# Performance work log

Measured on AMD Instinct MI355X. Metric: run time of the kernel, lower is better.

## Reference

```python
import jax, jax.numpy as jnp
import numpy as np

ATTRACTION_W = 1.0
REPULSION_W = 1.0
BETA_POS_W = 1.0
BETA_NEG_W = 0.5
K_INST = 256  # max number of distinct instance ids (slice ids)


def setup_inputs() -> dict:
    key = jax.random.key(0)
    B, N, D, K = 4, 65536, 256, K_INST
    k1, k2, k3 = jax.random.split(key, 3)
    beta = jax.random.normal(k1, (B, N, 1), jnp.float32)
    embed = jax.random.normal(k2, (B, N, D), jnp.float32)
    sid = jax.random.randint(k3, (B, N), -1, K)  # -1 = background
    # force exactly one condensation point per instance: hit i (<K) -> sid=i, is_cp
    sid = sid.at[:, :K].set(jnp.broadcast_to(jnp.arange(K), (B, K)))
    is_cp = jnp.zeros((B, N), bool).at[:, :K].set(True)
    return {"beta": beta, "embed": embed, "slice_id": sid, "is_cp": is_cp}


def _loss_single(beta, emb, sid, cp):
    # beta: (N,) logits, emb: (N,D), sid: (N,) int, cp: (N,) bool
    N = sid.shape[0]
    valid = sid >= 0
    cpv = cp & valid  # condensation points with a valid instance id
    # BCE-with-logits: target 1 -> softplus(-x), target 0 -> softplus(x)
    pos = jnp.sum(jnp.where(cpv, jax.nn.softplus(-beta), 0.0)) / jnp.maximum(cpv.sum(), 1)
    noncp = ~cp
    neg = jnp.sum(jnp.where(noncp, jax.nn.softplus(beta), 0.0)) / jnp.maximum(noncp.sum(), 1)
    beta_loss = BETA_POS_W * pos + BETA_NEG_W * neg

    # first CP hit index per instance (segment-min over CP hits), N = "no CP"
    sid_c = jnp.where(valid, sid, 0)
    idx = jnp.arange(N)
    first_cp = jnp.full((K_INST,), N, jnp.int32).at[sid_c].min(
        jnp.where(cpv, idx, N).astype(jnp.int32))
    has_cp = first_cp < N
    cp_emb = emb[jnp.minimum(first_cp, N - 1)]  # (K, D), garbage where no CP

    # attraction: sum over instances of mean ||emb - inst_cp||^2
    d2 = jnp.sum((emb - cp_emb[sid_c]) ** 2, axis=-1)  # (N,)
    w = valid & has_cp[sid_c]
    seg_sum = jnp.zeros((K_INST,), jnp.float32).at[sid_c].add(jnp.where(w, d2, 0.0))
    seg_cnt = jnp.zeros((K_INST,), jnp.float32).at[sid_c].add(w.astype(jnp.float32))
    attraction = jnp.sum(jnp.where(seg_cnt > 0, seg_sum / jnp.maximum(seg_cnt, 1.0), 0.0))
    attraction = attraction * ATTRACTION_W

    # repulsion: mean exp(-||cp_i - cp_j||^2) over all CP pairs (incl. diagonal)
    pd2 = jnp.sum((cp_emb[:, None, :] - cp_emb[None, :, :]) ** 2, axis=-1)  # (K,K)
    pmask = has_cp[:, None] & has_cp[None, :]
    M = has_cp.sum()
    rep = jnp.sum(jnp.where(pmask, jnp.exp(-pd2), 0.0)) / jnp.maximum(M * M, 1)
    rep = jnp.where(M > 1, rep * REPULSION_W, 0.0)

    loss = beta_loss + attraction + rep
    ok = (valid.sum() > 0) & (cpv.sum() > 0)
    return jnp.where(ok, loss, 0.0), ok


def reference(beta, embed, slice_id, is_cp):
    losses, oks = jax.vmap(_loss_single)(beta.squeeze(-1), embed, slice_id, is_cp)
    cnt = oks.sum()
    return jnp.where(cnt > 0, losses.sum() / jnp.maximum(cnt, 1), 0.0)
```

## Files before the change

kernel.cpp:

```cpp
#include <hip/hip_runtime.h>
#include <math.h>

#define K_INST 256
#define ATTRACTION_W 1.0f
#define REPULSION_W 1.0f
#define BETA_POS_W 1.0f
#define BETA_NEG_W 0.5f

typedef float f32x4 __attribute__((ext_vector_type(4)));
typedef int i32x4 __attribute__((ext_vector_type(4)));

__device__ inline float softplusf(float x) {
    return fmaxf(x, 0.f) + log1pf(expf(-fabsf(x)));
}

__device__ inline float waveReduceSumF(float v) {
    for (int o = 32; o; o >>= 1) v += __shfl_xor(v, o);
    return v;
}
__device__ inline int waveReduceSumI(int v) {
    for (int o = 32; o; o >>= 1) v += __shfl_xor(v, o);
    return v;
}

__global__ void stats_kernel(const float* __restrict__ beta,
                             const int* __restrict__ sid,
                             const int* __restrict__ is_cp,
                             int* fc_rev,
                             float* pos_sum, float* neg_sum,
                             int* seg_cnt,
                             int* cpv_cnt, int* noncp_cnt, int* valid_cnt,
                             int N) {
    int b = blockIdx.y;
    int base = (blockIdx.x * blockDim.x + threadIdx.x) * 4;
    const float* betaB = beta + (size_t)b * N;
    const int* sidB = sid + (size_t)b * N;
    const int* cpB = is_cp + (size_t)b * N;

    __shared__ int hist[K_INST];
    for (int k = threadIdx.x; k < K_INST; k += blockDim.x) hist[k] = 0;
    __syncthreads();

    i32x4 s4 = *(const i32x4*)(sidB + base);
    i32x4 c4 = *(const i32x4*)(cpB + base);
    f32x4 x4 = *(const f32x4*)(betaB + base);

    float pos = 0.f, neg = 0.f;
    int c_cpv = 0, c_non = 0, c_val = 0;
    #pragma unroll
    for (int e = 0; e < 4; ++e) {
        int s = s4[e], cp = c4[e];
        float x = x4[e];
        bool valid = s >= 0;
        bool cpv = cp && valid;
        if (valid) atomicAdd(&hist[s], 1);
        if (cpv) {
            pos += softplusf(-x);
            c_cpv++;
            atomicMax(&fc_rev[b * K_INST + s], N - (base + e));
        }
        if (!cp) {
            neg += softplusf(x);
            c_non++;
        }
        c_val += valid ? 1 : 0;
    }

    __shared__ float sf[2][4];
    __shared__ int si[3][4];
    pos = waveReduceSumF(pos);
    neg = waveReduceSumF(neg);
    c_cpv = waveReduceSumI(c_cpv);
    c_non = waveReduceSumI(c_non);
    c_val = waveReduceSumI(c_val);
    int wave = threadIdx.x >> 6, lane = threadIdx.x & 63;
    if (lane == 0) {
        sf[0][wave] = pos; sf[1][wave] = neg;
        si[0][wave] = c_cpv; si[1][wave] = c_non; si[2][wave] = c_val;
    }
    __syncthreads();
    if (threadIdx.x == 0) {
        float p = sf[0][0] + sf[0][1] + sf[0][2] + sf[0][3];
        float n = sf[1][0] + sf[1][1] + sf[1][2] + sf[1][3];
        int a = si[0][0] + si[0][1] + si[0][2] + si[0][3];
        int c = si[1][0] + si[1][1] + si[1][2] + si[1][3];
        int v = si[2][0] + si[2][1] + si[2][2] + si[2][3];
        if (p != 0.f) atomicAdd(&pos_sum[b], p);
        if (n != 0.f) atomicAdd(&neg_sum[b], n);
        if (a) atomicAdd(&cpv_cnt[b], a);
        if (c) atomicAdd(&noncp_cnt[b], c);
        if (v) atomicAdd(&valid_cnt[b], v);
    }
    for (int k = threadIdx.x; k < K_INST; k += blockDim.x) {
        int h = hist[k];
        if (h) atomicAdd(&seg_cnt[b * K_INST + k], h);
    }
}

__global__ void scatter_kernel(const int* __restrict__ sid,
                               const int* __restrict__ seg_cnt,
                               int* cursor, int* order, int N) {
    int b = blockIdx.y;
    int base = (blockIdx.x * blockDim.x + threadIdx.x) * 4;
    const int* sidB = sid + (size_t)b * N;
    int* orderB = order + (size_t)b * N;

    __shared__ int lhist[K_INST];
    __shared__ int lcnt[K_INST];
    __shared__ int lbase[K_INST];
    __shared__ int scanA[K_INST];
    __shared__ int scanB[K_INST];

    int t = threadIdx.x;
    lhist[t] = 0; lcnt[t] = 0;
    __syncthreads();

    i32x4 s4 = *(const i32x4*)(sidB + base);
    #pragma unroll
    for (int e = 0; e < 4; ++e) {
        if (s4[e] >= 0) atomicAdd(&lhist[s4[e]], 1);
    }
    __syncthreads();

    int myCnt = seg_cnt[b * K_INST + t];
    scanA[t] = myCnt;
    __syncthreads();
    int* src = scanA; int* dst = scanB;
    #pragma unroll
    for (int off = 1; off < K_INST; off <<= 1) {
        int v = src[t] + ((t >= off) ? src[t - off] : 0);
        dst[t] = v;
        __syncthreads();
        int* tmp = src; src = dst; dst = tmp;
    }
    int segStart = src[t] - myCnt;
    int h = lhist[t];
    lbase[t] = (h > 0) ? atomicAdd(&cursor[b * K_INST + t], h) : 0;
    __syncthreads();

    #pragma unroll
    for (int e = 0; e < 4; ++e) {
        int s = s4[e];
        if (s >= 0) {
            int r = atomicAdd(&lcnt[s], 1);
        }
    }
    scanA[t] = segStart;
    __syncthreads();
    lcnt[t] = 0;
    __syncthreads();
    #pragma unroll
    for (int e = 0; e < 4; ++e) {
        int s = s4[e];
        if (s >= 0) {
            int r = atomicAdd(&lcnt[s], 1);
            int slot = scanA[s] + lbase[s] + r;
            orderB[slot] = ((base + e) << 8) | s;
        }
    }
}

__global__ void gather_kernel(const float* __restrict__ embed,
                              const int* __restrict__ fc_rev,
                              float* __restrict__ cp_emb,
                              float* __restrict__ cp_embT, int N) {
    int b = blockIdx.y;
    int k = blockIdx.x;
    int src = N - fc_rev[b * K_INST + k];
    if (src >= N) src = N - 1;
    int lane = threadIdx.x;
    const float* embB = embed + (size_t)b * N * 256;
    f32x4 v = ((const f32x4*)(embB + (size_t)src * 256))[lane];
    ((f32x4*)(cp_emb + ((size_t)b * K_INST + k) * 256))[lane] = v;
    float* T = cp_embT + (size_t)b * K_INST * 256;
    int d = lane * 4;
    T[(size_t)(d + 0) * 256 + k] = v[0];
    T[(size_t)(d + 1) * 256 + k] = v[1];
    T[(size_t)(d + 2) * 256 + k] = v[2];
    T[(size_t)(d + 3) * 256 + k] = v[3];
}

__device__ inline float sel8f(const float* v, int lane) {
    float a0 = (lane & 1) ? v[1] : v[0];
    float a1 = (lane & 1) ? v[3] : v[2];
    float a2 = (lane & 1) ? v[5] : v[4];
    float a3 = (lane & 1) ? v[7] : v[6];
    float b0 = (lane & 2) ? a1 : a0;
    float b1 = (lane & 2) ? a3 : a2;
    return (lane & 4) ? b1 : b0;
}
__device__ inline int sel8i(const int* v, int lane) {
    int a0 = (lane & 1) ? v[1] : v[0];
    int a1 = (lane & 1) ? v[3] : v[2];
    int a2 = (lane & 1) ? v[5] : v[4];
    int a3 = (lane & 1) ? v[7] : v[6];
    int b0 = (lane & 2) ? a1 : a0;
    int b1 = (lane & 2) ? a3 : a2;
    return (lane & 4) ? b1 : b0;
}

__global__ void attraction_repulsion_kernel(
        const float* __restrict__ embed,
        const int* __restrict__ order,
        const int* __restrict__ fc_rev,
        const float* __restrict__ cp_emb,
        const float* __restrict__ cp_embT,
        float* seg_sum, float* rep_sum,
        int N, int atr_blocks) {
    int b = blockIdx.y;
    __shared__ __align__(16) char smem[8448];
    __shared__ float sf[4];

    const float* cpB = cp_emb + (size_t)b * K_INST * 256;

    if (blockIdx.x < 32) {
        float (*srow)[264] = (float(*)[264])smem;
        const int* fcB = fc_rev + b * K_INST;
        int i0 = blockIdx.x * 8;
        const float* T = cp_embT + (size_t)b * K_INST * 256;
        {
            int r = threadIdx.x >> 5, cc = (threadIdx.x & 31) * 8;
            f32x4 a = *(const f32x4*)(cpB + (size_t)(i0 + r) * 256 + cc);
            f32x4 bv = *(const f32x4*)(cpB + (size_t)(i0 + r) * 256 + cc + 4);
            srow[r][cc + 0] = a[0]; srow[r][cc + 1] = a[1];
            srow[r][cc + 2] = a[2]; srow[r][cc + 3] = a[3];
            srow[r][cc + 4] = bv[0]; srow[r][cc + 5] = bv[1];
            srow[r][cc + 6] = bv[2]; srow[r][cc + 7] = bv[3];
        }
        __syncthreads();

        int j = threadIdx.x;
        bool has_j = fcB[j] > 0;
        float acc[8] = {0.f, 0.f, 0.f, 0.f, 0.f, 0.f, 0.f, 0.f};
        for (int d = 0; d < 256; d += 2) {
            float v0 = T[(size_t)d * 256 + j];
            float v1 = T[(size_t)(d + 1) * 256 + j];
            #pragma unroll
            for (int r = 0; r < 8; ++r) {
                float f0 = srow[r][d] - v0;
                float f1 = srow[r][d + 1] - v1;
                acc[r] += f0 * f0 + f1 * f1;
            }
        }
        float val = 0.f;
        #pragma unroll
        for (int r = 0; r < 8; ++r) {
            bool has_i = fcB[i0 + r] > 0;
            if (has_i && has_j) val += expf(-acc[r]);
        }
        val = waveReduceSumF(val);
        int wave = threadIdx.x >> 6, lane = threadIdx.x & 63;
        if (lane == 0) sf[wave] = val;
        __syncthreads();
        if (threadIdx.x == 0)
            atomicAdd(&rep_sum[b], sf[0] + sf[1] + sf[2] + sf[3]);
    } else {
        float* s_sum = (float*)smem;
        for (int k = threadIdx.x; k < K_INST; k += blockDim.x) s_sum[k] = 0.f;
        __syncthreads();

        int bx = blockIdx.x - 32;
        int lane = threadIdx.x & 63;
        int wid = bx * 4 + (threadIdx.x >> 6);
        int stride = atr_blocks * 4 * 8;

        const float* embB = embed + (size_t)b * N * 256;
        const int* ordB = order + (size_t)b * N;

        int i = wid * 8;
        i32x4 ea = {-1, -1, -1, -1}, eb = {-1, -1, -1, -1};
        if (i < N) {
            ea = __builtin_nontemporal_load((const i32x4*)(ordB + i));
            eb = __builtin_nontemporal_load((const i32x4*)(ordB + i + 4));
        }
        while (i < N) {
            int en[8] = {ea[0], ea[1], ea[2], ea[3], eb[0], eb[1], eb[2], eb[3]};
            int ss[8];
            #pragma unroll
            for (int j = 0; j < 8; ++j) ss[j] = en[j] < 0 ? -1 : (en[j] & 255);

            f32x4 e[8];
            #pragma unroll
            for (int j = 0; j < 8; ++j) {
                int off = ((en[j] < 0 ? 0 : (en[j] >> 8)) << 8) | (lane << 2);
                e[j] = __builtin_nontemporal_load((const f32x4*)(embB + off));
            }
            f32x4 c[8];
            #pragma unroll
            for (int j = 0; j < 8; ++j) {
                int off = ((ss[j] < 0 ? 0 : ss[j]) << 8) | (lane << 2);
                c[j] = *(const f32x4*)(cpB + off);
            }
            int inext = i + stride;
            i32x4 na = {-1, -1, -1, -1}, nb = {-1, -1, -1, -1};
            if (inext < N) {
                na = __builtin_nontemporal_load((const i32x4*)(ordB + inext));
                nb = __builtin_nontemporal_load((const i32x4*)(ordB + inext + 4));
            }

            float v[8];
            #pragma unroll
            for (int j = 0; j < 8; ++j) {
                float d0 = e[j][0] - c[j][0], d1 = e[j][1] - c[j][1];
                float d2 = e[j][2] - c[j][2], d3 = e[j][3] - c[j][3];
                v[j] = d0 * d0 + d1 * d1 + d2 * d2 + d3 * d3;
            }
            #pragma unroll
            for (int o = 1; o <= 4; o <<= 1) {
                #pragma unroll
                for (int j = 0; j < 8; ++j) v[j] += __shfl_xor(v[j], o);
            }
            float w = sel8f(v, lane & 7);
            #pragma unroll
            for (int o = 8; o <= 32; o <<= 1) w += __shfl_xor(w, o);
            if (lane < 8) {
                int s_sel = sel8i(ss, lane);
                if (s_sel >= 0) atomicAdd(&s_sum[s_sel], w);
            }
            ea = na; eb = nb;
            i = inext;
        }
        __syncthreads();
        for (int k = threadIdx.x; k < K_INST; k += blockDim.x) {
            float v = s_sum[k];
            if (v != 0.f) atomicAdd(&seg_sum[b * K_INST + k], v);
        }
    }
}

__global__ void final_kernel(const int* __restrict__ fc_rev,
                             const float* __restrict__ seg_sum,
                             const int* __restrict__ seg_cnt,
                             const float* __restrict__ pos_sum,
                             const float* __restrict__ neg_sum,
                             const float* __restrict__ rep_sum,
                             const int* __restrict__ cpv_cnt,
                             const int* __restrict__ noncp_cnt,
                             const int* __restrict__ valid_cnt,
                             float* out, int N, int B) {
    __shared__ float s_att[4];
    __shared__ int s_m[4];
    float loss_sum = 0.f;
    int ok_cnt = 0;
    int wave = threadIdx.x >> 6, lane = threadIdx.x & 63;
    for (int b = 0; b < B; ++b) {
        int k = threadIdx.x;
        int has = (fc_rev[b * K_INST + k] > 0) ? 1 : 0;
        int cnt = seg_cnt[b * K_INST + k];
        float att = (has && cnt > 0) ? (seg_sum[b * K_INST + k] / (float)cnt) : 0.f;
        att = waveReduceSumF(att);
        has = waveReduceSumI(has);
        if (lane == 0) { s_att[wave] = att; s_m[wave] = has; }
        __syncthreads();
        if (threadIdx.x == 0) {
            float attraction = (s_att[0] + s_att[1] + s_att[2] + s_att[3]) * ATTRACTION_W;
            int M = s_m[0] + s_m[1] + s_m[2] + s_m[3];
            float pos = pos_sum[b] / fmaxf((float)cpv_cnt[b], 1.f);
            float neg = neg_sum[b] / fmaxf((float)noncp_cnt[b], 1.f);
            float beta_loss = BETA_POS_W * pos + BETA_NEG_W * neg;
            float rep = 0.f;
            if (M > 1) {
                float mm = (float)M * (float)M;
                rep = (rep_sum[b] / fmaxf(mm, 1.f)) * REPULSION_W;
            }
            float loss = beta_loss + attraction + rep;
            bool ok = (valid_cnt[b] > 0) && (cpv_cnt[b] > 0);
            if (ok) { loss_sum += loss; ok_cnt += 1; }
        }
        __syncthreads();
    }
    if (threadIdx.x == 0) {
        out[0] = (ok_cnt > 0) ? (loss_sum / (float)ok_cnt) : 0.f;
    }
}

extern "C" void kernel_launch(void* const* d_in, const int* in_sizes, int n_in,
                              void* d_out, int out_size, void* d_ws, size_t ws_size,
                              hipStream_t stream) {
    const float* beta  = (const float*)d_in[0];
    const float* embed = (const float*)d_in[1];
    const int* sid     = (const int*)d_in[2];
    const int* is_cp   = (const int*)d_in[3];
    float* out = (float*)d_out;

    const int N = 65536;
    const int B = in_sizes[0] / N;
    (void)n_in; (void)out_size; (void)ws_size;

    char* ws = (char*)d_ws;
    int*   fc_rev    = (int*)(ws + 0);
    float* seg_sum   = (float*)(ws + 4096);
    int*   seg_cnt   = (int*)(ws + 8192);
    int*   cursor    = (int*)(ws + 12288);
    float* pos_sum   = (float*)(ws + 16384);
    float* neg_sum   = (float*)(ws + 16448);
    float* rep_sum   = (float*)(ws + 16512);
    int*   cpv_cnt   = (int*)(ws + 16576);
    int*   noncp_cnt = (int*)(ws + 16640);
    int*   valid_cnt = (int*)(ws + 16704);
    int*   order     = (int*)(ws + 20480);
    float* cp_emb    = (float*)(ws + 20480 + (size_t)B * N * 4);
    float* cp_embT   = cp_emb + (size_t)B * K_INST * 256;

    hipMemsetAsync(ws, 0, 20480, stream);
    hipMemsetAsync(order, 0xFF, (size_t)B * N * 4, stream);

    stats_kernel<<<dim3(N / 1024, B), dim3(256), 0, stream>>>(
        beta, sid, is_cp, fc_rev, pos_sum, neg_sum, seg_cnt,
        cpv_cnt, noncp_cnt, valid_cnt, N);

    scatter_kernel<<<dim3(N / 1024, B), dim3(256), 0, stream>>>(
        sid, seg_cnt, cursor, order, N);

    gather_kernel<<<dim3(K_INST, B), dim3(64), 0, stream>>>(
        embed, fc_rev, cp_emb, cp_embT, N);

    const int atr_blocks = 512;
    attraction_repulsion_kernel<<<dim3(32 + atr_blocks, B), dim3(256), 0, stream>>>(
        embed, order, fc_rev, cp_emb, cp_embT,
        seg_sum, rep_sum, N, atr_blocks);

    final_kernel<<<dim3(1), dim3(256), 0, stream>>>(
        fc_rev, seg_sum, seg_cnt, pos_sum, neg_sum, rep_sum,
        cpv_cnt, noncp_cnt, valid_cnt, out, N, B);
}
```

Baseline: 105.0 us.

## Compute attraction per segment via sum and sum-of-squares expansion

Attraction is now computed with one block per instance. Each block walks that instance's sorted hit list and accumulates the vector sum and the sum of squares of the embeddings. The mean squared distance then comes from the expansion ||e||^2 - 2 e·c + ||c||^2, so no per-hit CP embedding load or shuffle reduction is needed. The repulsion blocks are widened to 512 threads covering 16 rows each, the order-buffer fill memset is removed, and the scatter kernel drops its second counting pass. The cost is possible load imbalance across segments, a short serial loop per wave, and cancellation error in float32 from the expanded form.

```diff
diff --git a/kernel.cpp b/kernel.cpp
--- a/kernel.cpp
+++ b/kernel.cpp
@@ -99,7 +99,7 @@
 
 __global__ void scatter_kernel(const int* __restrict__ sid,
                                const int* __restrict__ seg_cnt,
-                               int* cursor, int* order, int N) {
+                               int* cursor, int* order, int* seg_start, int N) {
     int b = blockIdx.y;
     int base = (blockIdx.x * blockDim.x + threadIdx.x) * 4;
     const int* sidB = sid + (size_t)b * N;
@@ -110,6 +110,7 @@
     __shared__ int lbase[K_INST];
     __shared__ int scanA[K_INST];
     __shared__ int scanB[K_INST];
+    __shared__ int segS[K_INST];
 
     int t = threadIdx.x;
     lhist[t] = 0; lcnt[t] = 0;
@@ -133,7 +134,8 @@
         __syncthreads();
         int* tmp = src; src = dst; dst = tmp;
     }
-    int segStart = src[t] - myCnt;
+    segS[t] = src[t] - myCnt;
+    if (blockIdx.x == 0) seg_start[b * K_INST + t] = segS[t];
     int h = lhist[t];
     lbase[t] = (h > 0) ? atomicAdd(&cursor[b * K_INST + t], h) : 0;
     __syncthreads();
@@ -143,18 +145,7 @@
         int s = s4[e];
         if (s >= 0) {
             int r = atomicAdd(&lcnt[s], 1);
-        }
-    }
-    scanA[t] = segStart;
-    __syncthreads();
-    lcnt[t] = 0;
-    __syncthreads();
-    #pragma unroll
-    for (int e = 0; e < 4; ++e) {
-        int s = s4[e];
-        if (s >= 0) {
-            int r = atomicAdd(&lcnt[s], 1);
-            int slot = scanA[s] + lbase[s] + r;
+            int slot = segS[s] + lbase[s] + r;
             orderB[slot] = ((base + e) << 8) | s;
         }
     }
@@ -180,56 +171,117 @@
     T[(size_t)(d + 3) * 256 + k] = v[3];
 }
 
-__device__ inline float sel8f(const float* v, int lane) {
-    float a0 = (lane & 1) ? v[1] : v[0];
-    float a1 = (lane & 1) ? v[3] : v[2];
-    float a2 = (lane & 1) ? v[5] : v[4];
-    float a3 = (lane & 1) ? v[7] : v[6];
-    float b0 = (lane & 2) ? a1 : a0;
-    float b1 = (lane & 2) ? a3 : a2;
-    return (lane & 4) ? b1 : b0;
-}
-__device__ inline int sel8i(const int* v, int lane) {
-    int a0 = (lane & 1) ? v[1] : v[0];
-    int a1 = (lane & 1) ? v[3] : v[2];
-    int a2 = (lane & 1) ? v[5] : v[4];
-    int a3 = (lane & 1) ? v[7] : v[6];
-    int b0 = (lane & 2) ? a1 : a0;
-    int b1 = (lane & 2) ? a3 : a2;
-    return (lane & 4) ? b1 : b0;
-}
-
 __global__ void attraction_repulsion_kernel(
         const float* __restrict__ embed,
         const int* __restrict__ order,
+        const int* __restrict__ seg_start,
+        const int* __restrict__ seg_cnt,
         const int* __restrict__ fc_rev,
         const float* __restrict__ cp_emb,
         const float* __restrict__ cp_embT,
-        float* seg_sum, float* rep_sum,
-        int N, int atr_blocks) {
+        float* seg_att, float* rep_sum, int N) {
     int b = blockIdx.y;
-    __shared__ __align__(16) char smem[8448];
-    __shared__ float sf[4];
-
+    __shared__ __align__(16) float smemF[16896 / 4 + 16];
     const float* cpB = cp_emb + (size_t)b * K_INST * 256;
 
-    if (blockIdx.x < 32) {
-        float (*srow)[264] = (float(*)[264])smem;
+    if (blockIdx.x < K_INST) {
+        int s = blockIdx.x;
+        int cnt = seg_cnt[b * K_INST + s];
+        float* vec_lds = smemF;
+        float* sq_lds = smemF + 256;
+        if (threadIdx.x < 256) vec_lds[threadIdx.x] = 0.f;
+        if (threadIdx.x == 256 % 512) ;
+        if (threadIdx.x == 0) *sq_lds = 0.f;
+        __syncthreads();
+
+        int wave = threadIdx.x >> 6;
+        int lane = threadIdx.x & 63;
+        if (cnt > 0) {
+            int start = seg_start[b * K_INST + s];
+            int chunk = (cnt + 7) >> 3;
+            int w0 = start + wave * chunk;
+            int w1 = min(w0 + chunk, start + cnt);
+            const int* ordB = order + (size_t)b * N;
+            const float* embB = embed + (size_t)b * N * 256;
+
+            f32x4 acc = {0.f, 0.f, 0.f, 0.f};
+            float sq = 0.f;
+            for (int p = w0; p < w1; p += 4) {
+                int n = w1 - p;
+                int e0 = ordB[p];
+                int e1 = (n > 1) ? ordB[p + 1] : -1;
+                int e2 = (n > 2) ? ordB[p + 2] : -1;
+                int e3 = (n > 3) ? ordB[p + 3] : -1;
+                f32x4 v0 = __builtin_nontemporal_load(
+                    (const f32x4*)(embB + ((size_t)(e0 >> 8) << 8) + lane * 4));
+                acc += v0;
+                sq += v0[0] * v0[0] + v0[1] * v0[1] + v0[2] * v0[2] + v0[3] * v0[3];
+                if (e1 >= 0) {
+                    f32x4 v = __builtin_nontemporal_load(
+                        (const f32x4*)(embB + ((size_t)(e1 >> 8) << 8) + lane * 4));
+                    acc += v;
+                    sq += v[0] * v[0] + v[1] * v[1] + v[2] * v[2] + v[3] * v[3];
+                }
+                if (e2 >= 0) {
+                    f32x4 v = __builtin_nontemporal_load(
+                        (const f32x4*)(embB + ((size_t)(e2 >> 8) << 8) + lane * 4));
+                    acc += v;
+                    sq += v[0] * v[0] + v[1] * v[1] + v[2] * v[2] + v[3] * v[3];
+                }
+                if (e3 >= 0) {
+                    f32x4 v = __builtin_nontemporal_load(
+                        (const f32x4*)(embB + ((size_t)(e3 >> 8) << 8) + lane * 4));
+                    acc += v;
+                    sq += v[0] * v[0] + v[1] * v[1] + v[2] * v[2] + v[3] * v[3];
+                }
+            }
+            atomicAdd(&vec_lds[lane * 4 + 0], acc[0]);
+            atomicAdd(&vec_lds[lane * 4 + 1], acc[1]);
+            atomicAdd(&vec_lds[lane * 4 + 2], acc[2]);
+            atomicAdd(&vec_lds[lane * 4 + 3], acc[3]);
+            sq = waveReduceSumF(sq);
+            if (lane == 0) atomicAdd(sq_lds, sq);
+        }
+        __syncthreads();
+        if (threadIdx.x < 64) {
+            float att = 0.f;
+            if (cnt > 0) {
+                int lane2 = threadIdx.x;
+                f32x4 v = *(const f32x4*)(vec_lds + lane2 * 4);
+                f32x4 c = *(const f32x4*)(cpB + (size_t)s * 256 + lane2 * 4);
+                float dp = v[0] * c[0] + v[1] * c[1] + v[2] * c[2] + v[3] * c[3];
+                float cn = c[0] * c[0] + c[1] * c[1] + c[2] * c[2] + c[3] * c[3];
+                #pragma unroll
+                for (int o = 1; o <= 32; o <<= 1) {
+                    dp += __shfl_xor(dp, o);
+                    cn += __shfl_xor(cn, o);
+                }
+                if (lane2 == 0) {
+                    float sqv = *sq_lds;
+                    att = (sqv - 2.f * dp + (float)cnt * cn) / (float)cnt;
+                }
+            }
+            if (threadIdx.x == 0) seg_att[b * K_INST + s] = att;
+        }
+    } else {
+        float (*srow)[264] = (float(*)[264])smemF;
+        float* sf = smemF + 16 * 264;
         const int* fcB = fc_rev + b * K_INST;
-        int i0 = blockIdx.x * 8;
+        int i0 = (blockIdx.x - K_INST) * 16;
         const float* T = cp_embT + (size_t)b * K_INST * 256;
         {
-            int r = threadIdx.x >> 5, cc = (threadIdx.x & 31) * 8;
-            f32x4 a = *(const f32x4*)(cpB + (size_t)(i0 + r) * 256 + cc);
-            f32x4 bv = *(const f32x4*)(cpB + (size_t)(i0 + r) * 256 + cc + 4);
-            srow[r][cc + 0] = a[0]; srow[r][cc + 1] = a[1];
-            srow[r][cc + 2] = a[2]; srow[r][cc + 3] = a[3];
-            srow[r][cc + 4] = bv[0]; srow[r][cc + 5] = bv[1];
-            srow[r][cc + 6] = bv[2]; srow[r][cc + 7] = bv[3];
-        }
-        __syncthreads();
-
-        int j = threadIdx.x;
+            int row = threadIdx.x >> 5, cc = (threadIdx.x & 31) * 8;
+            f32x4 a = *(const f32x4*)(cpB + (size_t)(i0 + row) * 256 + cc);
+            f32x4 bv = *(const f32x4*)(cpB + (size_t)(i0 + row) * 256 + cc + 4);
+            srow[row][cc + 0] = a[0]; srow[row][cc + 1] = a[1];
+            srow[row][cc + 2] = a[2]; srow[row][cc + 3] = a[3];
+            srow[row][cc + 4] = bv[0]; srow[row][cc + 5] = bv[1];
+            srow[row][cc + 6] = bv[2]; srow[row][cc + 7] = bv[3];
+        }
+        __syncthreads();
+
+        int j = threadIdx.x & 255;
+        int half = threadIdx.x >> 8;
         bool has_j = fcB[j] > 0;
         float acc[8] = {0.f, 0.f, 0.f, 0.f, 0.f, 0.f, 0.f, 0.f};
         for (int d = 0; d < 256; d += 2) {
@@ -237,99 +289,33 @@
             float v1 = T[(size_t)(d + 1) * 256 + j];
             #pragma unroll
             for (int r = 0; r < 8; ++r) {
-                float f0 = srow[r][d] - v0;
-                float f1 = srow[r][d + 1] - v1;
+                int row = half * 8 + r;
+                float f0 = srow[row][d] - v0;
+                float f1 = srow[row][d + 1] - v1;
                 acc[r] += f0 * f0 + f1 * f1;
             }
         }
         float val = 0.f;
         #pragma unroll
         for (int r = 0; r < 8; ++r) {
-            bool has_i = fcB[i0 + r] > 0;
+            bool has_i = fcB[i0 + half * 8 + r] > 0;
             if (has_i && has_j) val += expf(-acc[r]);
         }
         val = waveReduceSumF(val);
         int wave = threadIdx.x >> 6, lane = threadIdx.x & 63;
         if (lane == 0) sf[wave] = val;
         __syncthreads();
-        if (threadIdx.x == 0)
-            atomicAdd(&rep_sum[b], sf[0] + sf[1] + sf[2] + sf[3]);
-    } else {
-        float* s_sum = (float*)smem;
-        for (int k = threadIdx.x; k < K_INST; k += blockDim.x) s_sum[k] = 0.f;
-        __syncthreads();
-
-        int bx = blockIdx.x - 32;
-        int lane = threadIdx.x & 63;
-        int wid = bx * 4 + (threadIdx.x >> 6);
-        int stride = atr_blocks * 4 * 8;
-
-        const float* embB = embed + (size_t)b * N * 256;
-        const int* ordB = order + (size_t)b * N;
-
-        int i = wid * 8;
-        i32x4 ea = {-1, -1, -1, -1}, eb = {-1, -1, -1, -1};
-        if (i < N) {
-            ea = __builtin_nontemporal_load((const i32x4*)(ordB + i));
-            eb = __builtin_nontemporal_load((const i32x4*)(ordB + i + 4));
-        }
-        while (i < N) {
-            int en[8] = {ea[0], ea[1], ea[2], ea[3], eb[0], eb[1], eb[2], eb[3]};
-            int ss[8];
+        if (threadIdx.x == 0) {
+            float t = 0.f;
             #pragma unroll
-            for (int j = 0; j < 8; ++j) ss[j] = en[j] < 0 ? -1 : (en[j] & 255);
-
-            f32x4 e[8];
-            #pragma unroll
-            for (int j = 0; j < 8; ++j) {
-                int off = ((en[j] < 0 ? 0 : (en[j] >> 8)) << 8) | (lane << 2);
-                e[j] = __builtin_nontemporal_load((const f32x4*)(embB + off));
-            }
-            f32x4 c[8];
-            #pragma unroll
-            for (int j = 0; j < 8; ++j) {
-                int off = ((ss[j] < 0 ? 0 : ss[j]) << 8) | (lane << 2);
-                c[j] = *(const f32x4*)(cpB + off);
-            }
-            int inext = i + stride;
-            i32x4 na = {-1, -1, -1, -1}, nb = {-1, -1, -1, -1};
-            if (inext < N) {
-                na = __builtin_nontemporal_load((const i32x4*)(ordB + inext));
-                nb = __builtin_nontemporal_load((const i32x4*)(ordB + inext + 4));
-            }
-
-            float v[8];
-            #pragma unroll
-            for (int j = 0; j < 8; ++j) {
-                float d0 = e[j][0] - c[j][0], d1 = e[j][1] - c[j][1];
-                float d2 = e[j][2] - c[j][2], d3 = e[j][3] - c[j][3];
-                v[j] = d0 * d0 + d1 * d1 + d2 * d2 + d3 * d3;
-            }
-            #pragma unroll
-            for (int o = 1; o <= 4; o <<= 1) {
-                #pragma unroll
-                for (int j = 0; j < 8; ++j) v[j] += __shfl_xor(v[j], o);
-            }
-            float w = sel8f(v, lane & 7);
-            #pragma unroll
-            for (int o = 8; o <= 32; o <<= 1) w += __shfl_xor(w, o);
-            if (lane < 8) {
-                int s_sel = sel8i(ss, lane);
-                if (s_sel >= 0) atomicAdd(&s_sum[s_sel], w);
-            }
-            ea = na; eb = nb;
-            i = inext;
-        }
-        __syncthreads();
-        for (int k = threadIdx.x; k < K_INST; k += blockDim.x) {
-            float v = s_sum[k];
-            if (v != 0.f) atomicAdd(&seg_sum[b * K_INST + k], v);
+            for (int w = 0; w < 8; ++w) t += sf[w];
+            atomicAdd(&rep_sum[b], t);
         }
     }
 }
 
 __global__ void final_kernel(const int* __restrict__ fc_rev,
-                             const float* __restrict__ seg_sum,
+                             const float* __restrict__ seg_att,
                              const int* __restrict__ seg_cnt,
                              const float* __restrict__ pos_sum,
                              const float* __restrict__ neg_sum,
@@ -347,7 +333,7 @@
         int k = threadIdx.x;
         int has = (fc_rev[b * K_INST + k] > 0) ? 1 : 0;
         int cnt = seg_cnt[b * K_INST + k];
-        float att = (has && cnt > 0) ? (seg_sum[b * K_INST + k] / (float)cnt) : 0.f;
+        float att = (has && cnt > 0) ? seg_att[b * K_INST + k] : 0.f;
         att = waveReduceSumF(att);
         has = waveReduceSumI(has);
         if (lane == 0) { s_att[wave] = att; s_m[wave] = has; }
@@ -389,38 +375,37 @@
 
     char* ws = (char*)d_ws;
     int*   fc_rev    = (int*)(ws + 0);
-    float* seg_sum   = (float*)(ws + 4096);
-    int*   seg_cnt   = (int*)(ws + 8192);
-    int*   cursor    = (int*)(ws + 12288);
-    float* pos_sum   = (float*)(ws + 16384);
-    float* neg_sum   = (float*)(ws + 16448);
-    float* rep_sum   = (float*)(ws + 16512);
-    int*   cpv_cnt   = (int*)(ws + 16576);
-    int*   noncp_cnt = (int*)(ws + 16640);
-    int*   valid_cnt = (int*)(ws + 16704);
-    int*   order     = (int*)(ws + 20480);
-    float* cp_emb    = (float*)(ws + 20480 + (size_t)B * N * 4);
+    int*   seg_cnt   = (int*)(ws + 4096);
+    int*   cursor    = (int*)(ws + 8192);
+    int*   seg_start = (int*)(ws + 12288);
+    float* seg_att   = (float*)(ws + 16384);
+    float* pos_sum   = (float*)(ws + 20480);
+    float* neg_sum   = (float*)(ws + 20544);
+    float* rep_sum   = (float*)(ws + 20608);
+    int*   cpv_cnt   = (int*)(ws + 20672);
+    int*   noncp_cnt = (int*)(ws + 20736);
+    int*   valid_cnt = (int*)(ws + 20800);
+    int*   order     = (int*)(ws + 24576);
+    float* cp_emb    = (float*)(ws + 24576 + (size_t)B * N * 4);
     float* cp_embT   = cp_emb + (size_t)B * K_INST * 256;
 
-    hipMemsetAsync(ws, 0, 20480, stream);
-    hipMemsetAsync(order, 0xFF, (size_t)B * N * 4, stream);
+    hipMemsetAsync(ws, 0, 24576, stream);
 
     stats_kernel<<<dim3(N / 1024, B), dim3(256), 0, stream>>>(
         beta, sid, is_cp, fc_rev, pos_sum, neg_sum, seg_cnt,
         cpv_cnt, noncp_cnt, valid_cnt, N);
 
     scatter_kernel<<<dim3(N / 1024, B), dim3(256), 0, stream>>>(
-        sid, seg_cnt, cursor, order, N);
+        sid, seg_cnt, cursor, order, seg_start, N);
 
     gather_kernel<<<dim3(K_INST, B), dim3(64), 0, stream>>>(
         embed, fc_rev, cp_emb, cp_embT, N);
 
-    const int atr_blocks = 512;
-    attraction_repulsion_kernel<<<dim3(32 + atr_blocks, B), dim3(256), 0, stream>>>(
-        embed, order, fc_rev, cp_emb, cp_embT,
-        seg_sum, rep_sum, N, atr_blocks);
+    attraction_repulsion_kernel<<<dim3(K_INST + 16, B), dim3(512), 0, stream>>>(
+        embed, order, seg_start, seg_cnt, fc_rev, cp_emb, cp_embT,
+        seg_att, rep_sum, N);
 
     final_kernel<<<dim3(1), dim3(256), 0, stream>>>(
-        fc_rev, seg_sum, seg_cnt, pos_sum, neg_sum, rep_sum,
+        fc_rev, seg_att, seg_cnt, pos_sum, neg_sum, rep_sum,
         cpv_cnt, noncp_cnt, valid_cnt, out, N, B);
 }
```

Result: slower. 109.6 us (+4.3%).
